# Performance work log

Hardware: AMD Instinct MI355X
Metric: run time of the kernel (lower is better)

The kernel has to match this reference:

```python
import jax, jax.numpy as jnp
import numpy as np

B, L = 2, 1024
D_MODEL, D_STATE, HEADDIM, EXPAND = 512, 16, 64, 2
D_INNER = EXPAND * D_MODEL          # 1024
NHEADS = D_INNER // HEADDIM         # 16
DCONV = 4
NLAYERS = 6
FFN = 4 * D_MODEL                   # 2048
CONV_DIM = D_INNER + 2 * D_STATE    # 1056
D_IN_PROJ = 2 * D_INNER + 2 * D_STATE + NHEADS  # 2096


def _rms(x, w, eps):
    return x * jax.lax.rsqrt(jnp.mean(x * x, axis=-1, keepdims=True) + eps) * w


def _mamba2(u, W_in, conv_w, conv_b, A_log, Dh, dt_bias, norm_w, W_out):
    # u: (b, l, d_model). Standard Mamba2 block (ngroups=1).
    b, l, _ = u.shape
    zxbcdt = u @ W_in                                   # (b, l, D_IN_PROJ)
    z = zxbcdt[..., :D_INNER]
    xBC = zxbcdt[..., D_INNER:D_INNER + CONV_DIM]
    dt = jax.nn.softplus(zxbcdt[..., D_INNER + CONV_DIM:] + dt_bias)  # (b, l, h)
    # causal depthwise conv, kernel size DCONV
    xpad = jnp.pad(xBC, ((0, 0), (DCONV - 1, 0), (0, 0)))
    xconv = conv_b + sum(xpad[:, k:k + l, :] * conv_w[:, k] for k in range(DCONV))
    xBC = jax.nn.silu(xconv)
    xh = xBC[..., :D_INNER].reshape(b, l, NHEADS, HEADDIM)
    Bm = xBC[..., D_INNER:D_INNER + D_STATE]            # (b, l, n)
    Cm = xBC[..., D_INNER + D_STATE:]                   # (b, l, n)
    A = -jnp.exp(A_log)                                 # (h,)
    dA = jnp.exp(dt * A)                                # (b, l, h)
    dtx = dt[..., None] * xh                            # (b, l, h, p)

    def step(h, inp):
        dA_t, dtx_t, B_t, C_t = inp
        h = h * dA_t[:, :, None, None] + dtx_t[..., None] * B_t[:, None, None, :]
        y = jnp.einsum('bhpn,bn->bhp', h, C_t)
        return h, y

    xs = (jnp.moveaxis(dA, 1, 0), jnp.moveaxis(dtx, 1, 0),
          jnp.moveaxis(Bm, 1, 0), jnp.moveaxis(Cm, 1, 0))
    h0 = jnp.zeros((b, NHEADS, HEADDIM, D_STATE), u.dtype)
    _, ys = jax.lax.scan(step, h0, xs)                  # (l, b, h, p)
    y = jnp.moveaxis(ys, 0, 1) + Dh[None, None, :, None] * xh
    y = y.reshape(b, l, D_INNER) * jax.nn.silu(z)       # gated
    y = _rms(y, norm_w, 1e-5)
    return y @ W_out


def _forward(x, position_embedding, pixel_mask, W_in, conv_w, conv_b, A_log, D,
             dt_bias, mnorm_w, W_out, norm_ssm_w, ffn_w1, ffn_b1, ffn_w2, ffn_b2,
             norm_ffn_w, final_norm_w):
    mask = pixel_mask[..., None]
    for i in range(NLAYERS):
        h = _rms(x, norm_ssm_w[i], 1e-6)
        s = (h + position_embedding) * mask
        fwd = _mamba2(s, W_in[i, 0], conv_w[i, 0], conv_b[i, 0], A_log[i, 0],
                      D[i, 0], dt_bias[i, 0], mnorm_w[i, 0], W_out[i, 0])
        bwd = jnp.flip(_mamba2(jnp.flip(s, 1), W_in[i, 1], conv_w[i, 1], conv_b[i, 1],
                               A_log[i, 1], D[i, 1], dt_bias[i, 1], mnorm_w[i, 1],
                               W_out[i, 1]), 1)
        x = x + 0.5 * (fwd + bwd) * mask
        hf = _rms(x, norm_ffn_w[i], 1e-6)
        x = x + jax.nn.gelu(hf @ ffn_w1[i] + ffn_b1[i], approximate=False) @ ffn_w2[i] + ffn_b2[i]
    return _rms(x, final_norm_w, 1e-6)


def setup_inputs() -> dict:
    key = jax.random.key(0)
    ks = jax.random.split(key, 12)
    s = 0.02
    f32 = jnp.float32
    return {
        'x': jax.random.normal(ks[0], (B, L, D_MODEL), f32),
        'position_embedding': jax.random.normal(ks[1], (B, L, D_MODEL), f32),
        'pixel_mask': jnp.ones((B, L), f32),
        'W_in': s * jax.random.normal(ks[2], (NLAYERS, 2, D_MODEL, D_IN_PROJ), f32),
        'conv_w': 0.3 * jax.random.normal(ks[3], (NLAYERS, 2, CONV_DIM, DCONV), f32),
        'conv_b': jnp.zeros((NLAYERS, 2, CONV_DIM), f32),
        'A_log': jnp.log(jax.random.uniform(ks[4], (NLAYERS, 2, NHEADS), f32, 1.0, 16.0)),
        'D': jnp.ones((NLAYERS, 2, NHEADS), f32),
        'dt_bias': jax.random.uniform(ks[5], (NLAYERS, 2, NHEADS), f32, -4.0, -1.0),
        'mnorm_w': jnp.ones((NLAYERS, 2, D_INNER), f32),
        'W_out': s * jax.random.normal(ks[6], (NLAYERS, 2, D_INNER, D_MODEL), f32),
        'norm_ssm_w': jnp.ones((NLAYERS, D_MODEL), f32),
        'ffn_w1': s * jax.random.normal(ks[7], (NLAYERS, D_MODEL, FFN), f32),
        'ffn_b1': jnp.zeros((NLAYERS, FFN), f32),
        'ffn_w2': s * jax.random.normal(ks[8], (NLAYERS, FFN, D_MODEL), f32),
        'ffn_b2': jnp.zeros((NLAYERS, D_MODEL), f32),
        'norm_ffn_w': jnp.ones((NLAYERS, D_MODEL), f32),
        'final_norm_w': jnp.ones((D_MODEL,), f32),
    }


def reference(x, position_embedding, pixel_mask, W_in, conv_w, conv_b, A_log, D,
              dt_bias, mnorm_w, W_out, norm_ssm_w, ffn_w1, ffn_b1, ffn_w2, ffn_b2,
              norm_ffn_w, final_norm_w):
    return _forward(x, position_embedding, pixel_mask, W_in, conv_w, conv_b, A_log, D,
                    dt_bias, mnorm_w, W_out, norm_ssm_w, ffn_w1, ffn_b1, ffn_w2, ffn_b2,
                    norm_ffn_w, final_norm_w)
```

## Files before the change

kernel.cpp:

```cpp
#include <hip/hip_runtime.h>
#include <cstdint>
#include <cstddef>

typedef __bf16 bf16;
typedef __bf16 bf16x4 __attribute__((ext_vector_type(4)));
typedef __bf16 bf16x8 __attribute__((ext_vector_type(8)));
typedef float f32x4 __attribute__((ext_vector_type(4)));

#define L_SEQ   1024
#define DMODEL  512
#define DINNER  1024
#define DSTATE  16
#define NHEADS  16
#define HEADDIM 64
#define CONVDIM 1056
#define DINPROJ 2096
#define FFN_DIM 2048
#define ROWS    2048
#define CHUNK   64
#define NCHUNK  16

__device__ __forceinline__ float wave_sum(float v) {
#pragma unroll
  for (int off = 32; off; off >>= 1) v += __shfl_down(v, off, 64);
  return v;
}
__device__ __forceinline__ float silu_f(float x) { return x / (1.0f + expf(-x)); }

__global__ __launch_bounds__(128) void rms_kernel(
    const float* __restrict__ x, const float* __restrict__ w,
    const float* __restrict__ pe, const float* __restrict__ mask,
    bf16* __restrict__ outb)
{
  int r = blockIdx.x, t = threadIdx.x;
  float4 v = ((const float4*)(x + (size_t)r * DMODEL))[t];
  float ss = v.x*v.x + v.y*v.y + v.z*v.z + v.w*v.w;
  ss = wave_sum(ss);
  __shared__ float red[2];
  if ((t & 63) == 0) red[t >> 6] = ss;
  __syncthreads();
  float rs = 1.0f / sqrtf((red[0] + red[1]) * (1.0f / DMODEL) + 1e-6f);
  float4 wv = ((const float4*)w)[t];
  float4 p = ((const float4*)(pe + (size_t)r * DMODEL))[t];
  float m = mask[r];
  bf16x4 o;
  o[0] = (bf16)((v.x*rs*wv.x + p.x) * m);
  o[1] = (bf16)((v.y*rs*wv.y + p.y) * m);
  o[2] = (bf16)((v.z*rs*wv.z + p.z) * m);
  o[3] = (bf16)((v.w*rs*wv.w + p.w) * m);
  *(bf16x4*)&outb[(size_t)r * DMODEL + t * 4] = o;
}

__global__ __launch_bounds__(256) void transpose_all(
    const float* __restrict__ W_in, const float* __restrict__ W_out,
    const float* __restrict__ f1, const float* __restrict__ f2,
    bf16* __restrict__ TIN, bf16* __restrict__ TOUT,
    bf16* __restrict__ T1, bf16* __restrict__ T2)
{
  int bid = blockIdx.x;
  const float* src; bf16* dst; int K, N, k0, n0;
  if (bid < 12672) {
    int slice = bid / 1056, rem = bid % 1056;
    K = 512; N = 2096;
    k0 = (rem % 16) * 32; n0 = (rem / 16) * 32;
    src = W_in + (size_t)slice * K * N;  dst = TIN + (size_t)slice * N * K;
  } else if (bid < 18816) {
    int t2 = bid - 12672;
    int slice = t2 / 512, rem = t2 % 512;
    K = 1024; N = 512;
    k0 = (rem % 32) * 32; n0 = (rem / 32) * 32;
    src = W_out + (size_t)slice * K * N; dst = TOUT + (size_t)slice * N * K;
  } else if (bid < 24960) {
    int t3 = bid - 18816;
    int slice = t3 / 1024, rem = t3 % 1024;
    K = 512; N = 2048;
    k0 = (rem % 16) * 32; n0 = (rem / 16) * 32;
    src = f1 + (size_t)slice * K * N;    dst = T1 + (size_t)slice * N * K;
  } else {
    int t4 = bid - 24960;
    int slice = t4 / 1024, rem = t4 % 1024;
    K = 2048; N = 512;
    k0 = (rem % 64) * 32; n0 = (rem / 64) * 32;
    src = f2 + (size_t)slice * K * N;    dst = T2 + (size_t)slice * N * K;
  }
  __shared__ float tile[32][33];
  int tx = threadIdx.x & 31, ty = threadIdx.x >> 5;
#pragma unroll
  for (int i = 0; i < 4; i++) {
    int k = k0 + ty + 8*i, n = n0 + tx;
    tile[ty + 8*i][tx] = (k < K && n < N) ? src[(size_t)k * N + n] : 0.0f;
  }
  __syncthreads();
#pragma unroll
  for (int i = 0; i < 4; i++) {
    int n = n0 + ty + 8*i, k = k0 + tx;
    if (n < N && k < K) dst[(size_t)n * K + k] = (bf16)tile[tx][ty + 8*i];
  }
}

template<int BM, int BN, int FI, int FJ, int MODE>
__global__ __launch_bounds__(256) void gemm_tile(
    const bf16* __restrict__ A, const bf16* __restrict__ BT,
    float* __restrict__ Cf, bf16* __restrict__ Cb,
    int M, int N, int K, int lda, int ldb,
    long aOffz, long bOffz, long cOffz, int flipz,
    const float* __restrict__ bias)
{
  constexpr int TG = (BM + BN) * 4;
  constexpr int NI = TG / 256;

  int z = blockIdx.z;
  A  += (size_t)z * aOffz;
  BT += (size_t)z * bOffz;
  long coff = (size_t)z * cOffz;
  int doflip = (flipz && z == 1);

  __shared__ __align__(16) bf16 Tile[(BM + BN) * 32];
  bf16* As = Tile;
  bf16* Bs = Tile + BM * 32;

  int m0 = blockIdx.x * BM, n0 = blockIdx.y * BN;
  int t = threadIdx.x;
  int lane = t & 63, w = t >> 6;
  int wr = w >> 1, wc = w & 1;
  int lr = lane & 15, lq = lane >> 4;

  const bf16* gsrc[NI];
#pragma unroll
  for (int i = 0; i < NI; i++) {
    int g = w * (TG / 4) + i * 64 + lane;
    if (g < BM * 4) {
      int row = g >> 2, kp = g & 3;
      int gr = m0 + row;
      if (doflip) gr ^= (L_SEQ - 1);
      gsrc[i] = A + (size_t)gr * lda + kp * 8;
    } else {
      int g2 = g - BM * 4;
      int row = g2 >> 2, kp = g2 & 3;
      int gn = n0 + row; if (gn >= N) gn = N - 1;
      gsrc[i] = BT + (size_t)gn * ldb + kp * 8;
    }
  }

  f32x4 zf = {0.0f, 0.0f, 0.0f, 0.0f};
  f32x4 acc[FI][FJ];
#pragma unroll
  for (int i = 0; i < FI; i++)
#pragma unroll
    for (int j = 0; j < FJ; j++) acc[i][j] = zf;

  for (int k0 = 0; k0 < K; k0 += 32) {
#pragma unroll
    for (int i = 0; i < NI; i++) {
      int chunk = w * (TG / 4) + i * 64;
      __builtin_amdgcn_global_load_lds(
          (const __attribute__((address_space(1))) void*)(gsrc[i] + k0),
          (__attribute__((address_space(3))) void*)&Tile[chunk * 8],
          16, 0, 0);
    }
    __syncthreads();

    bf16x8 af[FI], bfv[FJ];
#pragma unroll
    for (int i = 0; i < FI; i++)
      af[i] = *(const bf16x8*)&As[(wr * 64 + i * 16 + lr) * 32 + lq * 8];
#pragma unroll
    for (int j = 0; j < FJ; j++)
      bfv[j] = *(const bf16x8*)&Bs[(wc * (BN / 2) + j * 16 + lr) * 32 + lq * 8];
#pragma unroll
    for (int i = 0; i < FI; i++)
#pragma unroll
      for (int j = 0; j < FJ; j++)
        acc[i][j] = __builtin_amdgcn_mfma_f32_16x16x32_bf16(af[i], bfv[j], acc[i][j], 0, 0, 0);
    __syncthreads();
  }

#pragma unroll
  for (int i = 0; i < FI; i++) {
    int growb = m0 + wr * 64 + i * 16 + lq * 4;
#pragma unroll
    for (int j = 0; j < FJ; j++) {
      int gcol = n0 + wc * (BN / 2) + j * 16 + lr;
      if (gcol >= N) continue;
#pragma unroll
      for (int rr = 0; rr < 4; rr++) {
        int grow = growb + rr;
        float v = acc[i][j][rr];
        if (MODE == 1) {
          v += bias[gcol];
          v = 0.5f * v * (1.0f + erff(v * 0.70710678118f));
          Cb[coff + (size_t)grow * N + gcol] = (bf16)v;
        } else if (MODE == 3) {
          Cb[coff + (size_t)grow * N + gcol] = (bf16)v;
          if (gcol >= DINNER + CONVDIM)
            Cf[(size_t)z * ROWS * 16 + (size_t)grow * 16 + (gcol - (DINNER + CONVDIM))] = v;
        } else {
          Cf[coff + (size_t)grow * N + gcol] = v;
        }
      }
    }
  }
}

__global__ __launch_bounds__(256) void convdt_kernel(
    const bf16* __restrict__ ZX, const float* __restrict__ DTRAW,
    bf16* __restrict__ XBCC, float* __restrict__ DT, float* __restrict__ DA,
    const float* __restrict__ conv_w, const float* __restrict__ conv_b,
    const float* __restrict__ dt_bias, const float* __restrict__ A_log)
{
  int r = blockIdx.x, dir = blockIdx.y;
  int l = r & (L_SEQ - 1);
  int t = threadIdx.x;
  const bf16* zx = ZX + (size_t)dir * ROWS * DINPROJ;
  const float* cw = conv_w + (size_t)dir * CONVDIM * 4;
  const float* cb = conv_b + (size_t)dir * CONVDIM;
  bf16* xo = XBCC + ((size_t)dir * ROWS + r) * CONVDIM;

  for (int ci = t; ci < CONVDIM / 4; ci += 256) {
    int c = ci * 4;
    f32x4 wch[4];
#pragma unroll
    for (int j = 0; j < 4; j++) wch[j] = *(const f32x4*)&cw[(c + j) * 4];
    f32x4 cbv = *(const f32x4*)&cb[c];
    float acc[4] = {cbv[0], cbv[1], cbv[2], cbv[3]};
#pragma unroll
    for (int k = 0; k < 4; k++) {
      int ls = l + k - 3;
      if (ls < 0) continue;
      bf16x4 iv = *(const bf16x4*)&zx[(size_t)(r + k - 3) * DINPROJ + DINNER + c];
#pragma unroll
      for (int j = 0; j < 4; j++) acc[j] += (float)iv[j] * wch[j][k];
    }
    bf16x4 o;
#pragma unroll
    for (int j = 0; j < 4; j++) o[j] = (bf16)silu_f(acc[j]);
    *(bf16x4*)&xo[c] = o;
  }
  if (t < NHEADS) {
    int h = t;
    float raw = DTRAW[((size_t)dir * ROWS + r) * 16 + h] + dt_bias[dir * NHEADS + h];
    float dt = (raw > 20.0f) ? raw : log1pf(expf(raw));
    float A = -expf(A_log[dir * NHEADS + h]);
    size_t idx = ((size_t)dir * ROWS + r) * NHEADS + h;
    DT[idx] = dt;
    DA[idx] = expf(dt * A);
  }
}

__global__ __launch_bounds__(64) void scan1_kernel(
    const bf16* __restrict__ XBCC, const float* __restrict__ DT,
    const float* __restrict__ DA, float* __restrict__ YSSM,
    float* __restrict__ HEND, float* __restrict__ APROD)
{
  int bid = blockIdx.x;
  int g = bid >> 4, c = bid & 15;
  int dir = g >> 5, rem = g & 31;
  int b = rem >> 4, h = rem & 15;
  int lane = threadIdx.x;
  size_t rowbase = (size_t)dir * ROWS + b * L_SEQ + c * CHUNK;
  const bf16* xb = XBCC + rowbase * CONVDIM;

  float dtv = DT[(rowbase + lane) * NHEADS + h];
  float dav = DA[(rowbase + lane) * NHEADS + h];

  float ap = dav;
#pragma unroll
  for (int off = 1; off < 64; off <<= 1) {
    float o = __shfl_up(ap, off, 64);
    if (lane >= off) ap *= o;
  }
  APROD[((size_t)g * NCHUNK + c) * 64 + lane] = ap;

  __shared__ float BCs[CHUNK][36];
#pragma unroll
  for (int i = 0; i < 8; i++) {
    int l = i * 8 + (lane >> 3), f = lane & 7;
    bf16x4 v = *(const bf16x4*)&xb[(size_t)l * CONVDIM + DINNER + f * 4];
#pragma unroll
    for (int q = 0; q < 4; q++) BCs[l][f * 4 + q] = (float)v[q];
  }
  __syncthreads();

  float hs[16];
#pragma unroll
  for (int n = 0; n < 16; n++) hs[n] = 0.0f;

  const bf16* xp = xb + h * HEADDIM + lane;
  float* yp = YSSM + rowbase * DINNER + h * HEADDIM + lane;

  for (int l = 0; l < CHUNK; l++) {
    float dt = __shfl(dtv, l, 64);
    float da = __shfl(dav, l, 64);
    float xv = (float)xp[(size_t)l * CONVDIM];
    float4 bq[4], cq[4];
#pragma unroll
    for (int q = 0; q < 4; q++) {
      bq[q] = *(const float4*)&BCs[l][q * 4];
      cq[q] = *(const float4*)&BCs[l][16 + q * 4];
    }
    const float* Bv = (const float*)bq;
    const float* Cv = (const float*)cq;
    float dtx = dt * xv;
    float acc = 0.0f;
#pragma unroll
    for (int n = 0; n < 16; n++) {
      hs[n] = hs[n] * da + dtx * Bv[n];
      acc += hs[n] * Cv[n];
    }
    yp[(size_t)l * DINNER] = acc;
  }

  float* he = HEND + ((size_t)g * NCHUNK + c) * 16 * 64;
#pragma unroll
  for (int n = 0; n < 16; n++) he[n * 64 + lane] = hs[n];
}

__global__ __launch_bounds__(64) void scan2_kernel(
    const bf16* __restrict__ XBCC, float* __restrict__ YSSM,
    const float* __restrict__ HEND, const float* __restrict__ APROD)
{
  int bid = blockIdx.x;
  int g = bid >> 4, c = bid & 15;
  if (c == 0) return;
  int dir = g >> 5, rem = g & 31;
  int b = rem >> 4, h = rem & 15;
  int lane = threadIdx.x;

  float hstart[16];
#pragma unroll
  for (int n = 0; n < 16; n++) hstart[n] = 0.0f;
  float w = 1.0f;
  for (int j = c - 1; j >= 0; j--) {
    const float* he = HEND + ((size_t)g * NCHUNK + j) * 16 * 64;
#pragma unroll
    for (int n = 0; n < 16; n++) hstart[n] += w * he[n * 64 + lane];
    w *= APROD[((size_t)g * NCHUNK + j) * 64 + 63];
  }

  size_t rowbase = (size_t)dir * ROWS + b * L_SEQ + c * CHUNK;
  const bf16* xb = XBCC + rowbase * CONVDIM;
  float* yp = YSSM + rowbase * DINNER + h * HEADDIM + lane;
  float apv = APROD[((size_t)g * NCHUNK + c) * 64 + lane];

  __shared__ float Cs[CHUNK][20];
#pragma unroll
  for (int i = 0; i < 4; i++) {
    int l = i * 16 + (lane >> 2), f = lane & 3;
    bf16x4 v = *(const bf16x4*)&xb[(size_t)l * CONVDIM + DINNER + 16 + f * 4];
#pragma unroll
    for (int q = 0; q < 4; q++) Cs[l][f * 4 + q] = (float)v[q];
  }
  __syncthreads();

  for (int l = 0; l < CHUNK; l++) {
    float a = __shfl(apv, l, 64);
    float4 cq[4];
#pragma unroll
    for (int q = 0; q < 4; q++) cq[q] = *(const float4*)&Cs[l][q * 4];
    const float* Cv = (const float*)cq;
    float acc = 0.0f;
#pragma unroll
    for (int n = 0; n < 16; n++) acc += Cv[n] * hstart[n];
    yp[(size_t)l * DINNER] += a * acc;
  }
}

__global__ __launch_bounds__(256) void gatenorm_kernel(
    const float* __restrict__ YSSM, const bf16* __restrict__ XBCC,
    const bf16* __restrict__ ZX, const float* __restrict__ Dparam,
    const float* __restrict__ mnorm_w, bf16* __restrict__ YB)
{
  int r = blockIdx.x, dir = blockIdx.y, t = threadIdx.x;
  const float* y = YSSM + ((size_t)dir * ROWS + r) * DINNER;
  const bf16* xb = XBCC + ((size_t)dir * ROWS + r) * CONVDIM;
  const bf16* z  = ZX   + ((size_t)dir * ROWS + r) * DINPROJ;
  int c = t * 4;
  int h = c >> 6;
  float Dv = Dparam[dir * NHEADS + h];
  float4 yv = *(const float4*)&y[c];
  bf16x4 xv4 = *(const bf16x4*)&xb[c];
  bf16x4 zv4 = *(const bf16x4*)&z[c];
  float val[4];
  val[0] = (yv.x + Dv*(float)xv4[0]) * silu_f((float)zv4[0]);
  val[1] = (yv.y + Dv*(float)xv4[1]) * silu_f((float)zv4[1]);
  val[2] = (yv.z + Dv*(float)xv4[2]) * silu_f((float)zv4[2]);
  val[3] = (yv.w + Dv*(float)xv4[3]) * silu_f((float)zv4[3]);
  float ss = val[0]*val[0] + val[1]*val[1] + val[2]*val[2] + val[3]*val[3];
  ss = wave_sum(ss);
  __shared__ float red[4];
  if ((t & 63) == 0) red[t >> 6] = ss;
  __syncthreads();
  float total = red[0] + red[1] + red[2] + red[3];
  float rs = 1.0f / sqrtf(total * (1.0f / DINNER) + 1e-5f);
  float4 wv = *(const float4*)&mnorm_w[dir * DINNER + c];
  bf16x4 o;
  o[0] = (bf16)(val[0] * rs * wv.x);
  o[1] = (bf16)(val[1] * rs * wv.y);
  o[2] = (bf16)(val[2] * rs * wv.z);
  o[3] = (bf16)(val[3] * rs * wv.w);
  *(bf16x4*)&YB[((size_t)dir * ROWS + r) * DINNER + c] = o;
}

__global__ __launch_bounds__(128) void combine_rms(
    const float* __restrict__ Xsrc, float* __restrict__ X,
    const float* __restrict__ P, const float* __restrict__ mask,
    const float* __restrict__ w, bf16* __restrict__ outb)
{
  int r = blockIdx.x, t = threadIdx.x;
  int b = r >> 10, l = r & 1023;
  int c = t * 4;
  float m = 0.5f * mask[r];
  float4 f = *(const float4*)&P[(size_t)r * DMODEL + c];
  size_t br = (size_t)ROWS * DMODEL + ((size_t)(b * L_SEQ + (L_SEQ - 1 - l))) * DMODEL + c;
  float4 bw = *(const float4*)&P[br];
  float4 x = *(const float4*)&Xsrc[(size_t)r * DMODEL + c];
  x.x += m * (f.x + bw.x);
  x.y += m * (f.y + bw.y);
  x.z += m * (f.z + bw.z);
  x.w += m * (f.w + bw.w);
  *(float4*)&X[(size_t)r * DMODEL + c] = x;
  float ss = x.x*x.x + x.y*x.y + x.z*x.z + x.w*x.w;
  ss = wave_sum(ss);
  __shared__ float red[2];
  if ((t & 63) == 0) red[t >> 6] = ss;
  __syncthreads();
  float rs = 1.0f / sqrtf((red[0] + red[1]) * (1.0f / DMODEL) + 1e-6f);
  float4 wv = *(const float4*)&w[c];
  bf16x4 o;
  o[0] = (bf16)(x.x * rs * wv.x);
  o[1] = (bf16)(x.y * rs * wv.y);
  o[2] = (bf16)(x.z * rs * wv.z);
  o[3] = (bf16)(x.w * rs * wv.w);
  *(bf16x4*)&outb[(size_t)r * DMODEL + c] = o;
}

__global__ __launch_bounds__(128) void reduce_rms(
    float* __restrict__ X, const float* __restrict__ P,
    const float* __restrict__ bias, const float* __restrict__ w,
    const float* __restrict__ pe, const float* __restrict__ mask,
    bf16* __restrict__ outb, float* __restrict__ outf)
{
  int r = blockIdx.x, t = threadIdx.x;
  int c = t * 4;
  float4 a  = *(const float4*)&P[(size_t)r * DMODEL + c];
  float4 b2 = *(const float4*)&P[(size_t)ROWS * DMODEL + (size_t)r * DMODEL + c];
  float4 bi = *(const float4*)&bias[c];
  float4 x  = *(float4*)&X[(size_t)r * DMODEL + c];
  x.x += a.x + b2.x + bi.x;
  x.y += a.y + b2.y + bi.y;
  x.z += a.z + b2.z + bi.z;
  x.w += a.w + b2.w + bi.w;
  *(float4*)&X[(size_t)r * DMODEL + c] = x;
  float ss = x.x*x.x + x.y*x.y + x.z*x.z + x.w*x.w;
  ss = wave_sum(ss);
  __shared__ float red[2];
  if ((t & 63) == 0) red[t >> 6] = ss;
  __syncthreads();
  float rs = 1.0f / sqrtf((red[0] + red[1]) * (1.0f / DMODEL) + 1e-6f);
  float4 wv = *(const float4*)&w[c];
  float4 o;
  o.x = x.x*rs*wv.x; o.y = x.y*rs*wv.y; o.z = x.z*rs*wv.z; o.w = x.w*rs*wv.w;
  if (pe) {
    float4 p = *(const float4*)&pe[(size_t)r * DMODEL + c];
    float m = mask[r];
    o.x = (o.x + p.x)*m; o.y = (o.y + p.y)*m; o.z = (o.z + p.z)*m; o.w = (o.w + p.w)*m;
  }
  if (outb) {
    bf16x4 ob = {(bf16)o.x, (bf16)o.y, (bf16)o.z, (bf16)o.w};
    *(bf16x4*)&outb[(size_t)r * DMODEL + c] = ob;
  } else {
    *(float4*)&outf[(size_t)r * DMODEL + c] = o;
  }
}

extern "C" void kernel_launch(void* const* d_in, const int* in_sizes, int n_in,
                              void* d_out, int out_size, void* d_ws, size_t ws_size,
                              hipStream_t stream)
{
  const float* in_x    = (const float*)d_in[0];
  const float* in_pe   = (const float*)d_in[1];
  const float* in_mask = (const float*)d_in[2];
  const float* W_in    = (const float*)d_in[3];
  const float* conv_w  = (const float*)d_in[4];
  const float* conv_b  = (const float*)d_in[5];
  const float* A_log   = (const float*)d_in[6];
  const float* Dparam  = (const float*)d_in[7];
  const float* dt_bias = (const float*)d_in[8];
  const float* mnorm_w = (const float*)d_in[9];
  const float* W_out   = (const float*)d_in[10];
  const float* nssm_w  = (const float*)d_in[11];
  const float* ffn_w1  = (const float*)d_in[12];
  const float* ffn_b1  = (const float*)d_in[13];
  const float* ffn_w2  = (const float*)d_in[14];
  const float* ffn_b2  = (const float*)d_in[15];
  const float* nffn_w  = (const float*)d_in[16];
  const float* final_w = (const float*)d_in[17];

  if (ws_size < 142802944) return;

  char* ws = (char*)d_ws;
  float* XBUF  = (float*)(ws + 0);
  bf16*  SBUF  = (bf16*) (ws + 4194304);
  bf16*  ZXb   = (bf16*) (ws + 6291456);
  float* DTRAW = (float*)(ws + 23461888);
  bf16*  XBCC  = (bf16*) (ws + 23724032);
  float* DTb   = (float*)(ws + 32374784);
  float* DAb   = (float*)(ws + 32636928);
  float* YSSM  = (float*)(ws + 32899072);
  bf16*  YB    = (bf16*) (ws + 49676288);
  float* DOUT2 = (float*)(ws + 58064896);
  bf16*  MID   = (bf16*) (ws + 66453504);
  float* HEND  = (float*)(ws + 74842112);
  float* APROD = (float*)(ws + 79036416);
  bf16*  WTINa = (bf16*) (ws + 79298560);
  bf16*  WTOUTa= (bf16*) (ws + 105054208);
  bf16*  WT1a  = (bf16*) (ws + 117637120);
  bf16*  WT2a  = (bf16*) (ws + 130220032);

  transpose_all<<<31104, 256, 0, stream>>>(W_in, W_out, ffn_w1, ffn_w2,
                                           WTINa, WTOUTa, WT1a, WT2a);
  rms_kernel<<<ROWS, 128, 0, stream>>>(in_x, nssm_w, in_pe, in_mask, SBUF);

  for (int layer = 0; layer < 6; layer++) {
    const bf16* WTIN  = WTINa  + (size_t)layer * 2 * DMODEL * DINPROJ;
    const bf16* WTOUT = WTOUTa + (size_t)layer * 2 * DINNER * DMODEL;
    const bf16* WT1   = WT1a   + (size_t)layer * DMODEL * FFN_DIM;
    const bf16* WT2   = WT2a   + (size_t)layer * FFN_DIM * DMODEL;

    gemm_tile<128, 128, 4, 4, 3><<<dim3(16, 17, 2), 256, 0, stream>>>(
        SBUF, WTIN, DTRAW, ZXb, ROWS, DINPROJ, DMODEL, DMODEL, DMODEL,
        0L, (long)DINPROJ * DMODEL, (long)ROWS * DINPROJ, 1, nullptr);
    convdt_kernel<<<dim3(ROWS, 2), 256, 0, stream>>>(
        ZXb, DTRAW, XBCC, DTb, DAb,
        conv_w + (size_t)layer * 2 * CONVDIM * 4, conv_b + (size_t)layer * 2 * CONVDIM,
        dt_bias + layer * 2 * NHEADS, A_log + layer * 2 * NHEADS);
    scan1_kernel<<<1024, 64, 0, stream>>>(XBCC, DTb, DAb, YSSM, HEND, APROD);
    scan2_kernel<<<1024, 64, 0, stream>>>(XBCC, YSSM, HEND, APROD);
    gatenorm_kernel<<<dim3(ROWS, 2), 256, 0, stream>>>(
        YSSM, XBCC, ZXb, Dparam + layer * 2 * NHEADS, mnorm_w + layer * 2 * DINNER, YB);
    gemm_tile<128, 64, 4, 2, 0><<<dim3(16, 8, 2), 256, 0, stream>>>(
        YB, WTOUT, DOUT2, nullptr, ROWS, DMODEL, DINNER, DINNER, DINNER,
        (long)ROWS * DINNER, (long)DMODEL * DINNER, (long)ROWS * DMODEL, 0, nullptr);
    combine_rms<<<ROWS, 128, 0, stream>>>(
        layer == 0 ? in_x : XBUF, XBUF, DOUT2, in_mask, nffn_w + layer * DMODEL, SBUF);

    gemm_tile<128, 128, 4, 4, 1><<<dim3(16, 16, 1), 256, 0, stream>>>(
        SBUF, WT1, nullptr, MID, ROWS, FFN_DIM, DMODEL, DMODEL, DMODEL,
        0L, 0L, 0L, 0, ffn_b1 + layer * FFN_DIM);
    gemm_tile<128, 64, 4, 2, 0><<<dim3(16, 8, 2), 256, 0, stream>>>(
        MID, WT2, DOUT2, nullptr, ROWS, DMODEL, 1024, FFN_DIM, FFN_DIM,
        1024L, 1024L, (long)ROWS * DMODEL, 0, nullptr);
    if (layer < 5) {
      reduce_rms<<<ROWS, 128, 0, stream>>>(
          XBUF, DOUT2, ffn_b2 + layer * DMODEL, nssm_w + (layer + 1) * DMODEL,
          in_pe, in_mask, SBUF, nullptr);
    } else {
      reduce_rms<<<ROWS, 128, 0, stream>>>(
          XBUF, DOUT2, ffn_b2 + layer * DMODEL, final_w,
          nullptr, nullptr, nullptr, (float*)d_out);
    }
  }
}
```

Before: 1.185 ms.

## Fuse depthwise conv and D-skip into scan, store SSM output in bf16

The causal depthwise conv for the x channels moves into scan1, which computes it on the fly from the projection output with a sliding register window. It also folds the D*x skip term into the SSM output, which is now stored as bf16. The separate conv kernel now only produces B/C in fp32 plus dt/dA, which removes the XBCC intermediate buffer and the fp32 YSSM traffic. The weight transpose uses 64x32 tiles with half the blocks, and the FFN-up GEMM switches to 128x64 tiles. Rounding the SSM output to bf16 before scan2 accumulates into it adds some precision loss.

```diff
diff --git a/kernel.cpp b/kernel.cpp
--- a/kernel.cpp
+++ b/kernel.cpp
@@ -59,42 +59,44 @@
 {
   int bid = blockIdx.x;
   const float* src; bf16* dst; int K, N, k0, n0;
-  if (bid < 12672) {
-    int slice = bid / 1056, rem = bid % 1056;
+  if (bid < 6336) {
+    int slice = bid / 528, rem = bid % 528;
     K = 512; N = 2096;
-    k0 = (rem % 16) * 32; n0 = (rem / 16) * 32;
+    k0 = (rem % 8) * 64; n0 = (rem / 8) * 32;
     src = W_in + (size_t)slice * K * N;  dst = TIN + (size_t)slice * N * K;
-  } else if (bid < 18816) {
-    int t2 = bid - 12672;
-    int slice = t2 / 512, rem = t2 % 512;
+  } else if (bid < 9408) {
+    int t2 = bid - 6336;
+    int slice = t2 / 256, rem = t2 % 256;
     K = 1024; N = 512;
-    k0 = (rem % 32) * 32; n0 = (rem / 32) * 32;
+    k0 = (rem % 16) * 64; n0 = (rem / 16) * 32;
     src = W_out + (size_t)slice * K * N; dst = TOUT + (size_t)slice * N * K;
-  } else if (bid < 24960) {
-    int t3 = bid - 18816;
-    int slice = t3 / 1024, rem = t3 % 1024;
+  } else if (bid < 12480) {
+    int t3 = bid - 9408;
+    int slice = t3 / 512, rem = t3 % 512;
     K = 512; N = 2048;
-    k0 = (rem % 16) * 32; n0 = (rem / 16) * 32;
+    k0 = (rem % 8) * 64; n0 = (rem / 8) * 32;
     src = f1 + (size_t)slice * K * N;    dst = T1 + (size_t)slice * N * K;
   } else {
-    int t4 = bid - 24960;
-    int slice = t4 / 1024, rem = t4 % 1024;
+    int t4 = bid - 12480;
+    int slice = t4 / 512, rem = t4 % 512;
     K = 2048; N = 512;
-    k0 = (rem % 64) * 32; n0 = (rem / 64) * 32;
+    k0 = (rem % 32) * 64; n0 = (rem / 32) * 32;
     src = f2 + (size_t)slice * K * N;    dst = T2 + (size_t)slice * N * K;
   }
-  __shared__ float tile[32][33];
-  int tx = threadIdx.x & 31, ty = threadIdx.x >> 5;
-#pragma unroll
-  for (int i = 0; i < 4; i++) {
-    int k = k0 + ty + 8*i, n = n0 + tx;
-    tile[ty + 8*i][tx] = (k < K && n < N) ? src[(size_t)k * N + n] : 0.0f;
-  }
-  __syncthreads();
-#pragma unroll
-  for (int i = 0; i < 4; i++) {
-    int n = n0 + ty + 8*i, k = k0 + tx;
-    if (n < N && k < K) dst[(size_t)n * K + k] = (bf16)tile[tx][ty + 8*i];
+  __shared__ float tile[64][33];
+  int nn = threadIdx.x & 31, kk = threadIdx.x >> 5;
+#pragma unroll
+  for (int i = 0; i < 8; i++) {
+    int k = kk + 8 * i, n = n0 + nn;
+    tile[k][nn] = (n < N) ? src[(size_t)(k0 + k) * N + n] : 0.0f;
+  }
+  __syncthreads();
+  int kk2 = threadIdx.x & 63, nn2 = threadIdx.x >> 6;
+#pragma unroll
+  for (int i = 0; i < 8; i++) {
+    int n = nn2 + 4 * i;
+    if (n0 + n < N)
+      dst[(size_t)(n0 + n) * K + k0 + kk2] = (bf16)tile[kk2][n];
   }
 }
 
@@ -202,42 +204,28 @@
   }
 }
 
-__global__ __launch_bounds__(256) void convdt_kernel(
+__global__ __launch_bounds__(64) void convdt_bc(
     const bf16* __restrict__ ZX, const float* __restrict__ DTRAW,
-    bf16* __restrict__ XBCC, float* __restrict__ DT, float* __restrict__ DA,
+    float* __restrict__ BCf, float* __restrict__ DT, float* __restrict__ DA,
     const float* __restrict__ conv_w, const float* __restrict__ conv_b,
     const float* __restrict__ dt_bias, const float* __restrict__ A_log)
 {
   int r = blockIdx.x, dir = blockIdx.y;
   int l = r & (L_SEQ - 1);
   int t = threadIdx.x;
-  const bf16* zx = ZX + (size_t)dir * ROWS * DINPROJ;
-  const float* cw = conv_w + (size_t)dir * CONVDIM * 4;
-  const float* cb = conv_b + (size_t)dir * CONVDIM;
-  bf16* xo = XBCC + ((size_t)dir * ROWS + r) * CONVDIM;
-
-  for (int ci = t; ci < CONVDIM / 4; ci += 256) {
-    int c = ci * 4;
-    f32x4 wch[4];
-#pragma unroll
-    for (int j = 0; j < 4; j++) wch[j] = *(const f32x4*)&cw[(c + j) * 4];
-    f32x4 cbv = *(const f32x4*)&cb[c];
-    float acc[4] = {cbv[0], cbv[1], cbv[2], cbv[3]};
+  if (t < 32) {
+    int ch = DINNER + t;
+    const float* cw = conv_w + ((size_t)dir * CONVDIM + ch) * 4;
+    float acc = conv_b[(size_t)dir * CONVDIM + ch];
+    const bf16* zc = ZX + (size_t)dir * ROWS * DINPROJ + DINNER + ch;
 #pragma unroll
     for (int k = 0; k < 4; k++) {
       int ls = l + k - 3;
-      if (ls < 0) continue;
-      bf16x4 iv = *(const bf16x4*)&zx[(size_t)(r + k - 3) * DINPROJ + DINNER + c];
-#pragma unroll
-      for (int j = 0; j < 4; j++) acc[j] += (float)iv[j] * wch[j][k];
-    }
-    bf16x4 o;
-#pragma unroll
-    for (int j = 0; j < 4; j++) o[j] = (bf16)silu_f(acc[j]);
-    *(bf16x4*)&xo[c] = o;
-  }
-  if (t < NHEADS) {
-    int h = t;
+      if (ls >= 0) acc += (float)zc[(size_t)(r + k - 3) * DINPROJ] * cw[k];
+    }
+    BCf[((size_t)dir * ROWS + r) * 32 + t] = silu_f(acc);
+  } else if (t < 48) {
+    int h = t - 32;
     float raw = DTRAW[((size_t)dir * ROWS + r) * 16 + h] + dt_bias[dir * NHEADS + h];
     float dt = (raw > 20.0f) ? raw : log1pf(expf(raw));
     float A = -expf(A_log[dir * NHEADS + h]);
@@ -248,9 +236,12 @@
 }
 
 __global__ __launch_bounds__(64) void scan1_kernel(
-    const bf16* __restrict__ XBCC, const float* __restrict__ DT,
-    const float* __restrict__ DA, float* __restrict__ YSSM,
-    float* __restrict__ HEND, float* __restrict__ APROD)
+    const bf16* __restrict__ ZX, const float* __restrict__ BCf,
+    const float* __restrict__ DT, const float* __restrict__ DA,
+    bf16* __restrict__ YSSM, float* __restrict__ HEND,
+    float* __restrict__ APROD,
+    const float* __restrict__ conv_w, const float* __restrict__ conv_b,
+    const float* __restrict__ Dparam)
 {
   int bid = blockIdx.x;
   int g = bid >> 4, c = bid & 15;
@@ -258,7 +249,6 @@
   int b = rem >> 4, h = rem & 15;
   int lane = threadIdx.x;
   size_t rowbase = (size_t)dir * ROWS + b * L_SEQ + c * CHUNK;
-  const bf16* xb = XBCC + rowbase * CONVDIM;
 
   float dtv = DT[(rowbase + lane) * NHEADS + h];
   float dav = DA[(rowbase + lane) * NHEADS + h];
@@ -275,23 +265,35 @@
 #pragma unroll
   for (int i = 0; i < 8; i++) {
     int l = i * 8 + (lane >> 3), f = lane & 7;
-    bf16x4 v = *(const bf16x4*)&xb[(size_t)l * CONVDIM + DINNER + f * 4];
-#pragma unroll
-    for (int q = 0; q < 4; q++) BCs[l][f * 4 + q] = (float)v[q];
-  }
-  __syncthreads();
+    float4 v = *(const float4*)&BCf[(rowbase + l) * 32 + f * 4];
+    *(float4*)&BCs[l][f * 4] = v;
+  }
+  __syncthreads();
+
+  int ch = h * HEADDIM + lane;
+  f32x4 cwv = *(const f32x4*)&conv_w[((size_t)dir * CONVDIM + ch) * 4];
+  float cbv = conv_b[(size_t)dir * CONVDIM + ch];
+  const bf16* xcol = ZX + rowbase * DINPROJ + DINNER + ch;
+  int lg0 = c * CHUNK;
+  float xm3 = (lg0 >= 3) ? (float)xcol[-3 * DINPROJ] : 0.0f;
+  float xm2 = (lg0 >= 2) ? (float)xcol[-2 * DINPROJ] : 0.0f;
+  float xm1 = (lg0 >= 1) ? (float)xcol[-1 * DINPROJ] : 0.0f;
+
+  float Dv = Dparam[dir * NHEADS + h];
 
   float hs[16];
 #pragma unroll
   for (int n = 0; n < 16; n++) hs[n] = 0.0f;
 
-  const bf16* xp = xb + h * HEADDIM + lane;
-  float* yp = YSSM + rowbase * DINNER + h * HEADDIM + lane;
+  bf16* yp = YSSM + rowbase * DINNER + ch;
 
   for (int l = 0; l < CHUNK; l++) {
     float dt = __shfl(dtv, l, 64);
     float da = __shfl(dav, l, 64);
-    float xv = (float)xp[(size_t)l * CONVDIM];
+    float xcur = (float)xcol[(size_t)l * DINPROJ];
+    float conv = cbv + cwv[0]*xm3 + cwv[1]*xm2 + cwv[2]*xm1 + cwv[3]*xcur;
+    xm3 = xm2; xm2 = xm1; xm1 = xcur;
+    float xv = silu_f(conv);
     float4 bq[4], cq[4];
 #pragma unroll
     for (int q = 0; q < 4; q++) {
@@ -307,7 +309,7 @@
       hs[n] = hs[n] * da + dtx * Bv[n];
       acc += hs[n] * Cv[n];
     }
-    yp[(size_t)l * DINNER] = acc;
+    yp[(size_t)l * DINNER] = (bf16)(acc + Dv * xv);
   }
 
   float* he = HEND + ((size_t)g * NCHUNK + c) * 16 * 64;
@@ -316,7 +318,7 @@
 }
 
 __global__ __launch_bounds__(64) void scan2_kernel(
-    const bf16* __restrict__ XBCC, float* __restrict__ YSSM,
+    const float* __restrict__ BCf, bf16* __restrict__ YSSM,
     const float* __restrict__ HEND, const float* __restrict__ APROD)
 {
   int bid = blockIdx.x;
@@ -338,17 +340,15 @@
   }
 
   size_t rowbase = (size_t)dir * ROWS + b * L_SEQ + c * CHUNK;
-  const bf16* xb = XBCC + rowbase * CONVDIM;
-  float* yp = YSSM + rowbase * DINNER + h * HEADDIM + lane;
+  bf16* yp = YSSM + rowbase * DINNER + h * HEADDIM + lane;
   float apv = APROD[((size_t)g * NCHUNK + c) * 64 + lane];
 
   __shared__ float Cs[CHUNK][20];
 #pragma unroll
   for (int i = 0; i < 4; i++) {
     int l = i * 16 + (lane >> 2), f = lane & 3;
-    bf16x4 v = *(const bf16x4*)&xb[(size_t)l * CONVDIM + DINNER + 16 + f * 4];
-#pragma unroll
-    for (int q = 0; q < 4; q++) Cs[l][f * 4 + q] = (float)v[q];
+    float4 v = *(const float4*)&BCf[(rowbase + l) * 32 + 16 + f * 4];
+    *(float4*)&Cs[l][f * 4] = v;
   }
   __syncthreads();
 
@@ -361,30 +361,25 @@
     float acc = 0.0f;
 #pragma unroll
     for (int n = 0; n < 16; n++) acc += Cv[n] * hstart[n];
-    yp[(size_t)l * DINNER] += a * acc;
+    float y = (float)yp[(size_t)l * DINNER];
+    yp[(size_t)l * DINNER] = (bf16)(y + a * acc);
   }
 }
 
 __global__ __launch_bounds__(256) void gatenorm_kernel(
-    const float* __restrict__ YSSM, const bf16* __restrict__ XBCC,
-    const bf16* __restrict__ ZX, const float* __restrict__ Dparam,
+    const bf16* __restrict__ YSSM, const bf16* __restrict__ ZX,
     const float* __restrict__ mnorm_w, bf16* __restrict__ YB)
 {
   int r = blockIdx.x, dir = blockIdx.y, t = threadIdx.x;
-  const float* y = YSSM + ((size_t)dir * ROWS + r) * DINNER;
-  const bf16* xb = XBCC + ((size_t)dir * ROWS + r) * CONVDIM;
-  const bf16* z  = ZX   + ((size_t)dir * ROWS + r) * DINPROJ;
+  const bf16* y = YSSM + ((size_t)dir * ROWS + r) * DINNER;
+  const bf16* z  = ZX  + ((size_t)dir * ROWS + r) * DINPROJ;
   int c = t * 4;
-  int h = c >> 6;
-  float Dv = Dparam[dir * NHEADS + h];
-  float4 yv = *(const float4*)&y[c];
-  bf16x4 xv4 = *(const bf16x4*)&xb[c];
+  bf16x4 yv4 = *(const bf16x4*)&y[c];
   bf16x4 zv4 = *(const bf16x4*)&z[c];
   float val[4];
-  val[0] = (yv.x + Dv*(float)xv4[0]) * silu_f((float)zv4[0]);
-  val[1] = (yv.y + Dv*(float)xv4[1]) * silu_f((float)zv4[1]);
-  val[2] = (yv.z + Dv*(float)xv4[2]) * silu_f((float)zv4[2]);
-  val[3] = (yv.w + Dv*(float)xv4[3]) * silu_f((float)zv4[3]);
+#pragma unroll
+  for (int q = 0; q < 4; q++)
+    val[q] = (float)yv4[q] * silu_f((float)zv4[q]);
   float ss = val[0]*val[0] + val[1]*val[1] + val[2]*val[2] + val[3]*val[3];
   ss = wave_sum(ss);
   __shared__ float red[4];
@@ -496,28 +491,28 @@
   const float* nffn_w  = (const float*)d_in[16];
   const float* final_w = (const float*)d_in[17];
 
-  if (ws_size < 142802944) return;
+  if (ws_size < 126287872) return;
 
   char* ws = (char*)d_ws;
   float* XBUF  = (float*)(ws + 0);
   bf16*  SBUF  = (bf16*) (ws + 4194304);
   bf16*  ZXb   = (bf16*) (ws + 6291456);
   float* DTRAW = (float*)(ws + 23461888);
-  bf16*  XBCC  = (bf16*) (ws + 23724032);
-  float* DTb   = (float*)(ws + 32374784);
-  float* DAb   = (float*)(ws + 32636928);
-  float* YSSM  = (float*)(ws + 32899072);
-  bf16*  YB    = (bf16*) (ws + 49676288);
-  float* DOUT2 = (float*)(ws + 58064896);
-  bf16*  MID   = (bf16*) (ws + 66453504);
-  float* HEND  = (float*)(ws + 74842112);
-  float* APROD = (float*)(ws + 79036416);
-  bf16*  WTINa = (bf16*) (ws + 79298560);
-  bf16*  WTOUTa= (bf16*) (ws + 105054208);
-  bf16*  WT1a  = (bf16*) (ws + 117637120);
-  bf16*  WT2a  = (bf16*) (ws + 130220032);
-
-  transpose_all<<<31104, 256, 0, stream>>>(W_in, W_out, ffn_w1, ffn_w2,
+  float* BCf   = (float*)(ws + 23724032);
+  float* DTb   = (float*)(ws + 24248320);
+  float* DAb   = (float*)(ws + 24510464);
+  bf16*  YSSMb = (bf16*) (ws + 24772608);
+  bf16*  YB    = (bf16*) (ws + 33161216);
+  float* DOUT2 = (float*)(ws + 41549824);
+  bf16*  MID   = (bf16*) (ws + 49938432);
+  float* HEND  = (float*)(ws + 58327040);
+  float* APROD = (float*)(ws + 62521344);
+  bf16*  WTINa = (bf16*) (ws + 62783488);
+  bf16*  WTOUTa= (bf16*) (ws + 88539136);
+  bf16*  WT1a  = (bf16*) (ws + 101122048);
+  bf16*  WT2a  = (bf16*) (ws + 113704960);
+
+  transpose_all<<<15552, 256, 0, stream>>>(W_in, W_out, ffn_w1, ffn_w2,
                                            WTINa, WTOUTa, WT1a, WT2a);
   rms_kernel<<<ROWS, 128, 0, stream>>>(in_x, nssm_w, in_pe, in_mask, SBUF);
 
@@ -526,25 +521,28 @@
     const bf16* WTOUT = WTOUTa + (size_t)layer * 2 * DINNER * DMODEL;
     const bf16* WT1   = WT1a   + (size_t)layer * DMODEL * FFN_DIM;
     const bf16* WT2   = WT2a   + (size_t)layer * FFN_DIM * DMODEL;
+    const float* cw_l = conv_w + (size_t)layer * 2 * CONVDIM * 4;
+    const float* cb_l = conv_b + (size_t)layer * 2 * CONVDIM;
 
     gemm_tile<128, 128, 4, 4, 3><<<dim3(16, 17, 2), 256, 0, stream>>>(
         SBUF, WTIN, DTRAW, ZXb, ROWS, DINPROJ, DMODEL, DMODEL, DMODEL,
         0L, (long)DINPROJ * DMODEL, (long)ROWS * DINPROJ, 1, nullptr);
-    convdt_kernel<<<dim3(ROWS, 2), 256, 0, stream>>>(
-        ZXb, DTRAW, XBCC, DTb, DAb,
-        conv_w + (size_t)layer * 2 * CONVDIM * 4, conv_b + (size_t)layer * 2 * CONVDIM,
+    convdt_bc<<<dim3(ROWS, 2), 64, 0, stream>>>(
+        ZXb, DTRAW, BCf, DTb, DAb, cw_l, cb_l,
         dt_bias + layer * 2 * NHEADS, A_log + layer * 2 * NHEADS);
-    scan1_kernel<<<1024, 64, 0, stream>>>(XBCC, DTb, DAb, YSSM, HEND, APROD);
-    scan2_kernel<<<1024, 64, 0, stream>>>(XBCC, YSSM, HEND, APROD);
+    scan1_kernel<<<1024, 64, 0, stream>>>(
+        ZXb, BCf, DTb, DAb, YSSMb, HEND, APROD, cw_l, cb_l,
+        Dparam + layer * 2 * NHEADS);
+    scan2_kernel<<<1024, 64, 0, stream>>>(BCf, YSSMb, HEND, APROD);
     gatenorm_kernel<<<dim3(ROWS, 2), 256, 0, stream>>>(
-        YSSM, XBCC, ZXb, Dparam + layer * 2 * NHEADS, mnorm_w + layer * 2 * DINNER, YB);
+        YSSMb, ZXb, mnorm_w + layer * 2 * DINNER, YB);
     gemm_tile<128, 64, 4, 2, 0><<<dim3(16, 8, 2), 256, 0, stream>>>(
         YB, WTOUT, DOUT2, nullptr, ROWS, DMODEL, DINNER, DINNER, DINNER,
         (long)ROWS * DINNER, (long)DMODEL * DINNER, (long)ROWS * DMODEL, 0, nullptr);
     combine_rms<<<ROWS, 128, 0, stream>>>(
         layer == 0 ? in_x : XBUF, XBUF, DOUT2, in_mask, nffn_w + layer * DMODEL, SBUF);
 
-    gemm_tile<128, 128, 4, 4, 1><<<dim3(16, 16, 1), 256, 0, stream>>>(
+    gemm_tile<128, 64, 4, 2, 1><<<dim3(16, 32, 1), 256, 0, stream>>>(
         SBUF, WT1, nullptr, MID, ROWS, FFN_DIM, DMODEL, DMODEL, DMODEL,
         0L, 0L, 0L, 0, ffn_b1 + layer * FFN_DIM);
     gemm_tile<128, 64, 4, 2, 0><<<dim3(16, 8, 2), 256, 0, stream>>>(
```

Result: faster. 1.077 ms (-9.1%).
